# Kernel tuning notes

Hardware: AMD Instinct MI355X
Metric: run time of the kernel (lower is better)

The kernel has to match this reference:

```python
import jax, jax.numpy as jnp
import numpy as np

H = 16  # num_attention_heads
D = 64  # attention_head_size


def setup_inputs() -> dict:
    key = jax.random.key(0)
    ks = jax.random.split(key, 10)
    B, S, Hid = 8, 512, 1024
    scale = 0.02
    hidden_states = jax.random.normal(ks[0], (B, S, Hid), jnp.float32)
    attention_mask = jnp.zeros((B, 1, 1, S), jnp.float32)
    graph_emb = jax.random.randint(ks[1], (B, S, S), 0, 3, jnp.int32)
    Wq = jax.random.normal(ks[2], (Hid, Hid), jnp.float32) * scale
    bq = jnp.zeros((Hid,), jnp.float32)
    Wk = jax.random.normal(ks[3], (Hid, Hid), jnp.float32) * scale
    bk = jnp.zeros((Hid,), jnp.float32)
    Wv = jax.random.normal(ks[4], (Hid, Hid), jnp.float32) * scale
    bv = jnp.zeros((Hid,), jnp.float32)
    dp_k = jax.random.normal(ks[5], (3, D), jnp.float32) * scale
    dp_v = jax.random.normal(ks[6], (3, D), jnp.float32) * scale
    return {"hidden_states": hidden_states, "attention_mask": attention_mask,
            "graph_emb": graph_emb, "Wq": Wq, "bq": bq, "Wk": Wk, "bk": bk,
            "Wv": Wv, "bv": bv, "dp_k": dp_k, "dp_v": dp_v}


def reference(hidden_states, attention_mask, graph_emb, Wq, bq, Wk, bk, Wv, bv, dp_k, dp_v):
    B, S, Hid = hidden_states.shape

    def proj(W, b):  # nn.Linear: x @ W.T + b, then split heads -> [B,H,S,D]
        y = hidden_states @ W.T + b
        return y.reshape(B, S, H, D).transpose(0, 2, 1, 3)

    q = proj(Wq, bq)
    k = proj(Wk, bk)
    v = proj(Wv, bv)

    # padding_idx=0 -> row 0 of relation tables is zero
    dp_k = dp_k.at[0].set(0.0)
    dp_v = dp_v.at[0].set(0.0)
    dp_keys = dp_k[graph_emb]    # [B,S,S,D]
    dp_values = dp_v[graph_emb]  # [B,S,S,D]

    scores = jnp.einsum('bhqd,bhkd->bhqk', q, k) / jnp.sqrt(jnp.float32(D))
    scores = scores + jnp.einsum('bhqd,bqkd->bhqk', q, dp_keys)  # relative_matmul_dp
    scores = scores + attention_mask
    probs = jax.nn.softmax(scores, axis=-1)

    ctx = jnp.einsum('bhqk,bhkd->bhqd', probs, v)
    ctx = ctx + jnp.einsum('bhqk,bqkd->bhqd', probs, dp_values)  # relative_matmul_dpv
    return ctx.transpose(0, 2, 1, 3).reshape(B, S, H * D)
```

## Files before the change

kernel.cpp:

```cpp
#include <hip/hip_runtime.h>
#include <hip/hip_bf16.h>
#include <cstddef>

#define B_  8
#define S_  512
#define HID 1024
#define H_  16
#define D_  64

typedef float f32x4 __attribute__((ext_vector_type(4)));
typedef _Float16 f16x8 __attribute__((ext_vector_type(8)));
typedef short s16x8 __attribute__((ext_vector_type(8)));
typedef unsigned short u16t;

__device__ __forceinline__ u16t f2h(float v) {
    return __builtin_bit_cast(u16t, (_Float16)v);
}
__device__ __forceinline__ float h2f(u16t u) {
    return (float)__builtin_bit_cast(_Float16, u);
}

__device__ __forceinline__ void gll16(const u16t* g, u16t* l) {
    __builtin_amdgcn_global_load_lds(
        (const __attribute__((address_space(1))) unsigned int*)(const void*)g,
        (__attribute__((address_space(3))) unsigned int*)(void*)l, 16, 0, 0);
}

__global__ __launch_bounds__(256) void conv_all_kernel(
    const float* __restrict__ X,
    const float* __restrict__ Wq, const float* __restrict__ Wk,
    const float* __restrict__ Wv,
    u16t* __restrict__ Xh, u16t* __restrict__ Wh)
{
    const int nX4 = (B_ * S_ * HID) / 4;
    const int nW4 = (HID * HID) / 4;
    int i = blockIdx.x * 256 + threadIdx.x;
    const float* src;
    u16t* dst;
    int off;
    if (i < nX4)                { src = X;  dst = Xh;                         off = i; }
    else if (i < nX4 + nW4)     { src = Wq; dst = Wh;                         off = i - nX4; }
    else if (i < nX4 + 2 * nW4) { src = Wk; dst = Wh + (size_t)HID * HID;     off = i - nX4 - nW4; }
    else                        { src = Wv; dst = Wh + (size_t)2 * HID * HID; off = i - nX4 - 2 * nW4; }
    float4 x = ((const float4*)src)[off];
    ushort4 h;
    h.x = f2h(x.x);
    h.y = f2h(x.y);
    h.z = f2h(x.z);
    h.w = f2h(x.w);
    ((ushort4*)dst)[off] = h;
}

__global__ __launch_bounds__(256) void qkv_mfma_kernel(
    const u16t* __restrict__ Xhi, const u16t* __restrict__ Whi,
    const float* __restrict__ bq, const float* __restrict__ bk,
    const float* __restrict__ bv,
    u16t* __restrict__ Qh, u16t* __restrict__ Kh, u16t* __restrict__ Vth)
{
    const int which = blockIdx.z;
    const u16t* __restrict__ WhiB = Whi + (size_t)which * (HID * HID);
    const float* __restrict__ bias = (which == 0) ? bq : (which == 1) ? bk : bv;

    __shared__ __align__(16) u16t SM[2 * 16384];

    const int tid  = threadIdx.x;
    const int lane = tid & 63;
    const int wv_  = tid >> 6;
    const int wr   = wv_ >> 1;
    const int wc   = wv_ & 1;
    const int m0   = blockIdx.y * 128;
    const int n0   = blockIdx.x * 128;

    f32x4 acc[4][4];
    #pragma unroll
    for (int mi = 0; mi < 4; ++mi)
        #pragma unroll
        for (int ni = 0; ni < 4; ++ni)
            #pragma unroll
            for (int e = 0; e < 4; ++e) acc[mi][ni][e] = 0.0f;

    const int rowB0 = wv_ * 32 + (lane >> 3);
    const int ch    = (lane & 7) ^ (rowB0 & 7);
    const size_t aof = (size_t)(m0 + rowB0) * HID + ch * 8;
    const size_t bof = (size_t)(n0 + rowB0) * HID + ch * 8;
    const int ldsA = (wv_ * 32) * 64;

    const int colL = lane & 15;
    const int kg   = lane >> 4;
    const int sx   = colL & 7;
    const int arow = (wr * 64 + colL) * 64;
    const int brow = (wc * 64 + colL) * 64;

    #pragma unroll
    for (int s = 0; s < 4; ++s) {
        gll16(&Xhi [aof + (size_t)(s * 8) * HID], SM + ldsA + s * 512);
        gll16(&WhiB[bof + (size_t)(s * 8) * HID], SM + 8192 + ldsA + s * 512);
    }
    __syncthreads();

    for (int k0 = 0; k0 < HID; k0 += 64) {
        const int cur = (k0 >> 6) & 1;
        u16t* const bufc = SM + cur * 16384;
        if (k0 + 64 < HID) {
            u16t* const bufn = SM + (cur ^ 1) * 16384;
            #pragma unroll
            for (int s = 0; s < 4; ++s) {
                gll16(&Xhi [aof + k0 + 64 + (size_t)(s * 8) * HID], bufn + ldsA + s * 512);
                gll16(&WhiB[bof + k0 + 64 + (size_t)(s * 8) * HID], bufn + 8192 + ldsA + s * 512);
            }
        }

        #pragma unroll
        for (int ks = 0; ks < 2; ++ks) {
            const int so = ((ks * 4 + kg) ^ sx) * 8;
            f16x8 a_[4], b_[4];
            #pragma unroll
            for (int mi = 0; mi < 4; ++mi)
                a_[mi] = *(const f16x8*)&bufc[arow + mi * 1024 + so];
            #pragma unroll
            for (int ni = 0; ni < 4; ++ni)
                b_[ni] = *(const f16x8*)&bufc[8192 + brow + ni * 1024 + so];
            #pragma unroll
            for (int mi = 0; mi < 4; ++mi)
                #pragma unroll
                for (int ni = 0; ni < 4; ++ni)
                    acc[mi][ni] = __builtin_amdgcn_mfma_f32_16x16x32_f16(
                        a_[mi], b_[ni], acc[mi][ni], 0, 0, 0);
        }
        __syncthreads();
    }

    if (which == 2) {
        #pragma unroll
        for (int mi = 0; mi < 4; ++mi) {
            #pragma unroll
            for (int ni = 0; ni < 4; ++ni) {
                const int n    = n0 + wc * 64 + ni * 16 + colL;
                const int mrow = m0 + wr * 64 + mi * 16 + kg * 4;
                const float bn = bias[n];
                const int bb = mrow >> 9;
                const int ss = mrow & (S_ - 1);
                const int hh = n >> 6;
                const int dd = n & (D_ - 1);
                ushort4 vh;
                vh.x = f2h(acc[mi][ni][0] + bn);
                vh.y = f2h(acc[mi][ni][1] + bn);
                vh.z = f2h(acc[mi][ni][2] + bn);
                vh.w = f2h(acc[mi][ni][3] + bn);
                *(ushort4*)&Vth[(((size_t)bb * H_ + hh) * D_ + dd) * S_ + ss] = vh;
            }
        }
    } else {
        u16t* __restrict__ Oh = (which == 0) ? Qh : Kh;
        float* LF = (float*)SM;
        float bn4[4];
        #pragma unroll
        for (int ni = 0; ni < 4; ++ni) bn4[ni] = bias[n0 + wc * 64 + ni * 16 + colL];

        const int er  = tid >> 3;
        const int ecc = (tid & 7) * 16;
        const int ehh = (n0 + ecc) >> 6;
        const int edd = ecc & 63;
        const int mrowE = m0 + (er >> 4) * 64 + (er & 15);

        #pragma unroll
        for (int mi = 0; mi < 4; ++mi) {
            __syncthreads();
            #pragma unroll
            for (int ni = 0; ni < 4; ++ni)
                #pragma unroll
                for (int j = 0; j < 4; ++j)
                    LF[(wr * 16 + kg * 4 + j) * 130 + wc * 64 + ni * 16 + colL] =
                        acc[mi][ni][j] + bn4[ni];
            __syncthreads();

            const int mrow = mrowE + mi * 16;
            const int bb = mrow >> 9;
            const int ss = mrow & (S_ - 1);
            __align__(16) u16t hv[16];
            #pragma unroll
            for (int u = 0; u < 16; u += 4) {
                float4 v = *(const float4*)&LF[er * 130 + ecc + u];
                hv[u + 0] = f2h(v.x);
                hv[u + 1] = f2h(v.y);
                hv[u + 2] = f2h(v.z);
                hv[u + 3] = f2h(v.w);
            }
            const size_t off = (((size_t)bb * H_ + ehh) * S_ + ss) * D_ + edd;
            *(s16x8*)&Oh[off]     = *(const s16x8*)&hv[0];
            *(s16x8*)&Oh[off + 8] = *(const s16x8*)&hv[8];
        }
    }
}

__global__ __launch_bounds__(512) void attn_mfma_kernel(
    const u16t* __restrict__ Qhg, const u16t* __restrict__ Khg,
    const u16t* __restrict__ Vhg,
    const int*  __restrict__ ge,  const float* __restrict__ mask,
    const float* __restrict__ dpk, const float* __restrict__ dpv,
    float* __restrict__ out)
{
    __shared__ __align__(16) u16t SM[24576];

    const int tid  = threadIdx.x;
    const int lane = tid & 63;
    const int wq   = tid >> 6;
    const int c    = lane & 15;
    const int g    = lane >> 4;
    const int sx   = c & 7;
    const int bid  = blockIdx.x;
    const int bh   = bid >> 2;
    const int q0   = (bid & 3) * 128;
    const int b    = bh >> 4;
    const int h    = bh & (H_ - 1);

    u16t* Pw = SM + 16384 + wq * 1024;

    const int qrow = q0 + wq * 16 + c;
    const size_t qoff = ((size_t)bh * S_ + qrow) * D_;
    const f16x8 qA = *(const f16x8*)&Qhg[qoff + g * 8];
    const f16x8 qB = *(const f16x8*)&Qhg[qoff + (g + 4) * 8];

    float tq1, tq2;
    {
        float a1 = 0.f, a2 = 0.f;
        #pragma unroll
        for (int i = 0; i < 8; ++i) {
            const float x0 = (float)qA[i];
            const float x1 = (float)qB[i];
            a1 = fmaf(x0, dpk[D_ + g * 8 + i], a1);
            a1 = fmaf(x1, dpk[D_ + (g + 4) * 8 + i], a1);
            a2 = fmaf(x0, dpk[2 * D_ + g * 8 + i], a2);
            a2 = fmaf(x1, dpk[2 * D_ + (g + 4) * 8 + i], a2);
        }
        a1 += __shfl_xor(a1, 16); a1 += __shfl_xor(a1, 32);
        a2 += __shfl_xor(a2, 16); a2 += __shfl_xor(a2, 32);
        tq1 = a1; tq2 = a2;
    }

    const int r_   = tid >> 3;
    const int s_   = tid & 7;
    const int ldso = r_ * 64 + ((s_ ^ (r_ & 7)) << 3);
    const u16t* kgp = &Khg[((size_t)bh * S_ + r_) * D_ + s_ * 8];
    const u16t* vgp = &Vhg[((size_t)bh * D_ + r_) * S_ + s_ * 8];

    s16x8 krS = *(const s16x8*)kgp;
    s16x8 vrS = *(const s16x8*)vgp;

    const size_t geoff = ((size_t)b * S_ + qrow) * S_;
    const float* mrow = &mask[(size_t)b * S_];

    float mrun = -INFINITY, lrun = 0.f, w1 = 0.f, w2 = 0.f;
    f32x4 ctx4[4];
    #pragma unroll
    for (int mi = 0; mi < 4; ++mi)
        #pragma unroll
        for (int e = 0; e < 4; ++e) ctx4[mi][e] = 0.f;

    for (int kt = 0; kt < S_ / 64; ++kt) {
        const int k0 = kt * 64;
        const int bufo = (kt & 1) << 13;
        u16t* const Kb = SM + bufo;
        u16t* const Vb = SM + bufo + 4096;

        *(s16x8*)&Kb[ldso] = krS;
        *(s16x8*)&Vb[ldso] = vrS;

        if (kt < S_ / 64 - 1) {
            krS = *(const s16x8*)(kgp + (size_t)(k0 + 64) * D_);
            vrS = *(const s16x8*)(vgp + (k0 + 64));
        }
        int4   gc4[4];
        float4 mk4[4];
        #pragma unroll
        for (int mi = 0; mi < 4; ++mi) {
            gc4[mi] = *(const int4*)&ge[geoff + k0 + mi * 16 + g * 4];
            mk4[mi] = *(const float4*)&mrow[k0 + mi * 16 + g * 4];
        }

        __syncthreads();

        f32x4 s4[4];
        #pragma unroll
        for (int mi = 0; mi < 4; ++mi)
            #pragma unroll
            for (int e = 0; e < 4; ++e) s4[mi][e] = 0.f;

        __builtin_amdgcn_s_setprio(1);
        #pragma unroll
        for (int ks = 0; ks < 2; ++ks) {
            const int so = ((g + 4 * ks) ^ sx) << 3;
            const f16x8 qh_ = ks ? qB : qA;
            #pragma unroll
            for (int mi = 0; mi < 4; ++mi) {
                const f16x8 kh_ = *(const f16x8*)&Kb[(mi * 16 + c) * 64 + so];
                s4[mi] = __builtin_amdgcn_mfma_f32_16x16x32_f16(kh_, qh_, s4[mi], 0, 0, 0);
            }
        }
        __builtin_amdgcn_s_setprio(0);

        float sv[4][4];
        int   gcode[4][4];
        float tmax = -INFINITY;
        #pragma unroll
        for (int mi = 0; mi < 4; ++mi) {
            const int   gg[4] = {gc4[mi].x, gc4[mi].y, gc4[mi].z, gc4[mi].w};
            const float mm[4] = {mk4[mi].x, mk4[mi].y, mk4[mi].z, mk4[mi].w};
            #pragma unroll
            for (int j = 0; j < 4; ++j) {
                const float t = (gg[j] == 1) ? tq1 : (gg[j] == 2) ? tq2 : 0.f;
                const float x = fmaf(s4[mi][j], 0.125f, t + mm[j]);
                sv[mi][j] = x;
                gcode[mi][j] = gg[j];
                tmax = fmaxf(tmax, x);
            }
        }
        tmax = fmaxf(tmax, __shfl_xor(tmax, 16));
        tmax = fmaxf(tmax, __shfl_xor(tmax, 32));

        if (!__all(tmax - mrun <= 8.0f)) {
            const float mn    = fmaxf(mrun, tmax);
            const float alpha = __expf(mrun - mn);
            mrun = mn;
            lrun *= alpha; w1 *= alpha; w2 *= alpha;
            #pragma unroll
            for (int mi = 0; mi < 4; ++mi) ctx4[mi] *= alpha;
        }

        float rs = 0.f, rb1 = 0.f, rb2 = 0.f;
        #pragma unroll
        for (int mi = 0; mi < 4; ++mi)
            #pragma unroll
            for (int j = 0; j < 4; ++j) {
                const float e = __expf(sv[mi][j] - mrun);
                sv[mi][j] = e;
                rs += e;
                rb1 += (gcode[mi][j] == 1) ? e : 0.f;
                rb2 += (gcode[mi][j] == 2) ? e : 0.f;
            }
        rs  += __shfl_xor(rs, 16);  rs  += __shfl_xor(rs, 32);
        rb1 += __shfl_xor(rb1, 16); rb1 += __shfl_xor(rb1, 32);
        rb2 += __shfl_xor(rb2, 16); rb2 += __shfl_xor(rb2, 32);

        lrun += rs;
        w1   += rb1;
        w2   += rb2;

        #pragma unroll
        for (int mi = 0; mi < 4; ++mi) {
            ushort4 ph;
            ph.x = f2h(sv[mi][0]);
            ph.y = f2h(sv[mi][1]);
            ph.z = f2h(sv[mi][2]);
            ph.w = f2h(sv[mi][3]);
            const int slotp = (2 * mi + (g >> 1)) ^ sx;
            *(ushort4*)&Pw[c * 64 + slotp * 8 + (g & 1) * 4] = ph;
        }

        __builtin_amdgcn_s_setprio(1);
        #pragma unroll
        for (int ks = 0; ks < 2; ++ks) {
            const int so = ((g + 4 * ks) ^ sx) << 3;
            const f16x8 ph_ = *(const f16x8*)&Pw[c * 64 + so];
            #pragma unroll
            for (int mi = 0; mi < 4; ++mi) {
                const f16x8 vh_ = *(const f16x8*)&Vb[(mi * 16 + c) * 64 + so];
                ctx4[mi] = __builtin_amdgcn_mfma_f32_16x16x32_f16(vh_, ph_, ctx4[mi], 0, 0, 0);
            }
        }
        __builtin_amdgcn_s_setprio(0);
    }

    __syncthreads();
    const float inv = 1.0f / lrun;
    float* tb = (float*)SM + wq * 1088;
    #pragma unroll
    for (int mi = 0; mi < 4; ++mi) {
        const float4 dk1 = *(const float4*)&dpv[D_ + mi * 16 + g * 4];
        const float4 dk2 = *(const float4*)&dpv[2 * D_ + mi * 16 + g * 4];
        const float a1[4] = {dk1.x, dk1.y, dk1.z, dk1.w};
        const float a2[4] = {dk2.x, dk2.y, dk2.z, dk2.w};
        #pragma unroll
        for (int j = 0; j < 4; ++j) {
            const float val = (ctx4[mi][j] + w1 * a1[j] + w2 * a2[j]) * inv;
            tb[(mi * 16 + g * 4 + j) * 17 + c] = val;
        }
    }
    __syncthreads();
    #pragma unroll
    for (int qq = 0; qq < 16; ++qq)
        out[((size_t)b * S_ + q0 + wq * 16 + qq) * (H_ * D_) + h * D_ + lane] =
            tb[lane * 17 + qq];
}

extern "C" void kernel_launch(void* const* d_in, const int* in_sizes, int n_in,
                              void* d_out, int out_size, void* d_ws, size_t ws_size,
                              hipStream_t stream)
{
    const float* hs   = (const float*)d_in[0];
    const float* mask = (const float*)d_in[1];
    const int*   ge   = (const int*)d_in[2];
    const float* Wq   = (const float*)d_in[3];
    const float* bq   = (const float*)d_in[4];
    const float* Wk   = (const float*)d_in[5];
    const float* bk   = (const float*)d_in[6];
    const float* Wv   = (const float*)d_in[7];
    const float* bv   = (const float*)d_in[8];
    const float* dpk  = (const float*)d_in[9];
    const float* dpv  = (const float*)d_in[10];
    float* out = (float*)d_out;

    const size_t per = (size_t)B_ * H_ * S_ * D_;
    const size_t nX  = (size_t)B_ * S_ * HID;
    const size_t nW  = (size_t)HID * HID;

    u16t* base = (u16t*)d_ws;
    u16t* Qh  = base;
    u16t* Kh  = Qh  + per;
    u16t* Vth = Kh  + per;
    u16t* Xhi = Vth + per;
    u16t* Whi = Xhi + nX;

    const int nConv = (int)((nX + 3 * nW) / 4);
    conv_all_kernel<<<nConv / 256, 256, 0, stream>>>(hs, Wq, Wk, Wv, Xhi, Whi);

    dim3 gridG(HID / 128, (B_ * S_) / 128, 3);
    qkv_mfma_kernel<<<gridG, dim3(256), 0, stream>>>(
        Xhi, Whi, bq, bk, bv, Qh, Kh, Vth);

    dim3 gridB(B_ * H_ * (S_ / 128));
    attn_mfma_kernel<<<gridB, dim3(512), 0, stream>>>(
        Qh, Kh, Vth, ge, mask, dpk, dpv, out);
}
```

Measured before the change: 78.02 us.

## Use four-stage K-pipeline with vmcnt waits in QKV projection GEMM

Restructures the QKV projection GEMM main loop from double-buffered 64-wide K tiles to a 4-deep ring of 32-wide K tiles. Loads are issued three stages ahead, with explicit s_waitcnt vmcnt counts and a single barrier per step, so that global-to-LDS latency overlaps with MFMA work. The LDS layout is re-swizzled to pair rows. The change adds more barriers per K (one per 32 elements) and depends on hand-counted waits being correct.

```diff
diff --git a/kernel.cpp b/kernel.cpp
--- a/kernel.cpp
+++ b/kernel.cpp
@@ -25,6 +25,10 @@
         (const __attribute__((address_space(1))) unsigned int*)(const void*)g,
         (__attribute__((address_space(3))) unsigned int*)(void*)l, 16, 0, 0);
 }
+
+#define WAITV8() asm volatile("s_waitcnt vmcnt(8)" ::: "memory")
+#define WAITV4() asm volatile("s_waitcnt vmcnt(4)" ::: "memory")
+#define WAITV0() asm volatile("s_waitcnt vmcnt(0)" ::: "memory")
 
 __global__ __launch_bounds__(256) void conv_all_kernel(
     const float* __restrict__ X,
@@ -61,7 +65,7 @@
     const u16t* __restrict__ WhiB = Whi + (size_t)which * (HID * HID);
     const float* __restrict__ bias = (which == 0) ? bq : (which == 1) ? bk : bv;
 
-    __shared__ __align__(16) u16t SM[2 * 16384];
+    __shared__ __align__(16) u16t SM[32768];
 
     const int tid  = threadIdx.x;
     const int lane = tid & 63;
@@ -70,6 +74,7 @@
     const int wc   = wv_ & 1;
     const int m0   = blockIdx.y * 128;
     const int n0   = blockIdx.x * 128;
+    const int NT   = HID / 32;
 
     f32x4 acc[4][4];
     #pragma unroll
@@ -79,56 +84,65 @@
             #pragma unroll
             for (int e = 0; e < 4; ++e) acc[mi][ni][e] = 0.0f;
 
-    const int rowB0 = wv_ * 32 + (lane >> 3);
-    const int ch    = (lane & 7) ^ (rowB0 & 7);
-    const size_t aof = (size_t)(m0 + rowB0) * HID + ch * 8;
-    const size_t bof = (size_t)(n0 + rowB0) * HID + ch * 8;
-    const int ldsA = (wv_ * 32) * 64;
+    const int c0 = tid, c1 = 256 + tid;
+    const int rp0 = c0 >> 3, u0 = (c0 & 7) ^ (rp0 & 7);
+    const int rp1 = c1 >> 3, u1 = (c1 & 7) ^ (rp1 & 7);
+    const size_t ga0 = (size_t)(m0 + 2 * rp0 + (u0 >> 2)) * HID + (u0 & 3) * 8;
+    const size_t ga1 = (size_t)(m0 + 2 * rp1 + (u1 >> 2)) * HID + (u1 & 3) * 8;
+    const size_t gb0 = (size_t)(n0 + 2 * rp0 + (u0 >> 2)) * HID + (u0 & 3) * 8;
+    const size_t gb1 = (size_t)(n0 + 2 * rp1 + (u1 >> 2)) * HID + (u1 & 3) * 8;
+    const int lA0 = wv_ * 512;
+    const int lA1 = 2048 + wv_ * 512;
 
     const int colL = lane & 15;
     const int kg   = lane >> 4;
-    const int sx   = colL & 7;
-    const int arow = (wr * 64 + colL) * 64;
-    const int brow = (wc * 64 + colL) * 64;
-
+    int aoffR[4], boffR[4];
     #pragma unroll
-    for (int s = 0; s < 4; ++s) {
-        gll16(&Xhi [aof + (size_t)(s * 8) * HID], SM + ldsA + s * 512);
-        gll16(&WhiB[bof + (size_t)(s * 8) * HID], SM + 8192 + ldsA + s * 512);
-    }
-    __syncthreads();
-
-    for (int k0 = 0; k0 < HID; k0 += 64) {
-        const int cur = (k0 >> 6) & 1;
-        u16t* const bufc = SM + cur * 16384;
-        if (k0 + 64 < HID) {
-            u16t* const bufn = SM + (cur ^ 1) * 16384;
-            #pragma unroll
-            for (int s = 0; s < 4; ++s) {
-                gll16(&Xhi [aof + k0 + 64 + (size_t)(s * 8) * HID], bufn + ldsA + s * 512);
-                gll16(&WhiB[bof + k0 + 64 + (size_t)(s * 8) * HID], bufn + 8192 + ldsA + s * 512);
-            }
-        }
-
-        #pragma unroll
-        for (int ks = 0; ks < 2; ++ks) {
-            const int so = ((ks * 4 + kg) ^ sx) * 8;
-            f16x8 a_[4], b_[4];
-            #pragma unroll
-            for (int mi = 0; mi < 4; ++mi)
-                a_[mi] = *(const f16x8*)&bufc[arow + mi * 1024 + so];
+    for (int mi = 0; mi < 4; ++mi) {
+        const int mrow = wr * 64 + mi * 16 + colL;
+        const int rp = mrow >> 1, hf = mrow & 1;
+        aoffR[mi] = rp * 64 + ((((hf << 2) | kg) ^ (rp & 7)) << 3);
+        const int nrow = wc * 64 + mi * 16 + colL;
+        const int rq = nrow >> 1, hg = nrow & 1;
+        boffR[mi] = rq * 64 + ((((hg << 2) | kg) ^ (rq & 7)) << 3);
+    }
+
+    #define STAGE_T(t) do {                                      \
+        u16t* bb_ = SM + ((t) & 3) * 8192;                       \
+        const size_t ko_ = (size_t)(t) * 32;                     \
+        gll16(&Xhi [ga0 + ko_], bb_ + lA0);                      \
+        gll16(&Xhi [ga1 + ko_], bb_ + lA1);                      \
+        gll16(&WhiB[gb0 + ko_], bb_ + 4096 + lA0);               \
+        gll16(&WhiB[gb1 + ko_], bb_ + 4096 + lA1);               \
+    } while (0)
+
+    STAGE_T(0);
+    STAGE_T(1);
+    STAGE_T(2);
+
+    for (int t = 0; t < NT; ++t) {
+        if (t < NT - 2)       WAITV8();
+        else if (t == NT - 2) WAITV4();
+        else                  WAITV0();
+        __builtin_amdgcn_s_barrier();
+        if (t + 3 < NT) STAGE_T(t + 3);
+
+        u16t* const bc = SM + (t & 3) * 8192;
+        f16x8 a_[4], b_[4];
+        #pragma unroll
+        for (int mi = 0; mi < 4; ++mi)
+            a_[mi] = *(const f16x8*)&bc[aoffR[mi]];
+        #pragma unroll
+        for (int ni = 0; ni < 4; ++ni)
+            b_[ni] = *(const f16x8*)&bc[4096 + boffR[ni]];
+        #pragma unroll
+        for (int mi = 0; mi < 4; ++mi)
             #pragma unroll
             for (int ni = 0; ni < 4; ++ni)
-                b_[ni] = *(const f16x8*)&bufc[8192 + brow + ni * 1024 + so];
-            #pragma unroll
-            for (int mi = 0; mi < 4; ++mi)
-                #pragma unroll
-                for (int ni = 0; ni < 4; ++ni)
-                    acc[mi][ni] = __builtin_amdgcn_mfma_f32_16x16x32_f16(
-                        a_[mi], b_[ni], acc[mi][ni], 0, 0, 0);
-        }
-        __syncthreads();
-    }
+                acc[mi][ni] = __builtin_amdgcn_mfma_f32_16x16x32_f16(
+                    a_[mi], b_[ni], acc[mi][ni], 0, 0, 0);
+    }
+    #undef STAGE_T
 
     if (which == 2) {
         #pragma unroll
```

Measured after the change: 80.54 us. 1.03x slower.
